# Optimization experiments

Measured on AMD Instinct MI355X. Metric: run time of the kernel, lower is better.

The kernel has to match this reference:

```python
import jax, jax.numpy as jnp
import numpy as np

EPS = 1e-6
NEG_SLOPE = 0.2


def knn_idx(xf, k):
    # xf: (B, C, N) flattened vector features; returns (B, N, k) neighbor indices
    xx = jnp.sum(xf * xf, axis=1)                       # (B, N)
    inner = jnp.einsum('bcn,bcm->bnm', xf, xf)          # (B, N, N)
    neg_dist = 2.0 * inner - xx[:, :, None] - xx[:, None, :]  # -||xi-xj||^2
    _, idx = jax.lax.top_k(neg_dist, k)                 # includes self (dist 0)
    return idx


def get_graph_feature(x, k):
    # x: (B, D, 3, N) -> edge features (B, 2D, 3, N, k)
    B, D, _, N = x.shape
    idx = knn_idx(x.reshape(B, D * 3, N), k)            # (B, N, k)
    pts = jnp.transpose(x, (0, 3, 1, 2))                # (B, N, D, 3)
    neigh = jax.vmap(lambda p, i: p[i])(pts, idx)       # (B, N, k, D, 3) gather
    center = jnp.broadcast_to(pts[:, :, None], neigh.shape)
    feat = jnp.concatenate([neigh - center, center], axis=3)  # (B, N, k, 2D, 3)
    return jnp.transpose(feat, (0, 3, 4, 1, 2))


def vn_linear_leakyrelu(x, Wf, Wd):
    # Vector-Neuron linear + leaky ReLU. x: (B, Cin, 3, ...),
    # Wf: (Cout, Cin), Wd: (Cout, Cin) or (1, Cin) when nonlinearity is shared.
    p = jnp.einsum('oi,bi...->bo...', Wf, x)
    d = jnp.einsum('oi,bi...->bo...', Wd, x)
    dot = jnp.sum(p * d, axis=2, keepdims=True)
    dsq = jnp.sum(d * d, axis=2, keepdims=True)
    proj = p - (dot / (dsq + EPS)) * d
    return NEG_SLOPE * p + (1.0 - NEG_SLOPE) * jnp.where(dot >= 0, p, proj)


def setup_inputs() -> dict:
    key = jax.random.key(0)
    ks = jax.random.split(key, 11)
    B, N = 8, 1024
    x = jax.random.normal(ks[0], (B, 3, N), dtype=jnp.float32)
    # dims = [1, 21, 21, 42, 85, 341]
    ins = [2, 42, 42, 84, 169]      # 2*dim_in for edge layers; sum(dims[1:-1]) for last
    outs = [21, 21, 42, 85, 341]
    dirs = [21, 21, 42, 85, 1]      # last layer has share_nonlinearity=True
    d = {"x": x}
    for i, (ci, co, cd) in enumerate(zip(ins, outs, dirs)):
        s = 1.0 / np.sqrt(ci)
        kf, kd = jax.random.split(ks[1 + i])
        d[f"Wf{i}"] = (jax.random.normal(kf, (co, ci), dtype=jnp.float32) * s)
        d[f"Wd{i}"] = (jax.random.normal(kd, (cd, ci), dtype=jnp.float32) * s)
    d["k"] = 20
    return d


def reference(x, Wf0, Wd0, Wf1, Wd1, Wf2, Wd2, Wf3, Wd3, Wf4, Wd4, k):
    cur = x[:, None]                 # (B, 1, 3, N)
    feats = []
    for Wf, Wd in ((Wf0, Wd0), (Wf1, Wd1), (Wf2, Wd2), (Wf3, Wd3)):
        g = get_graph_feature(cur, k)        # (B, 2D, 3, N, k)
        h = vn_linear_leakyrelu(g, Wf, Wd)   # (B, Dout, 3, N, k)
        cur = h.mean(axis=-1)                # mean over neighbors -> (B, Dout, 3, N)
        feats.append(cur)
    xcat = jnp.concatenate(feats, axis=1)    # (B, 169, 3, N)
    out = vn_linear_leakyrelu(xcat, Wf4, Wd4)
    return out.mean(axis=-1)                 # mean over points -> (B, 341, 3)
```

## Files before the change

kernel.cpp:

```cpp
#include <hip/hip_runtime.h>
#include <cstddef>

#define BB 8
#define NN 1024
#define KK 20
#define CCAT 169
#define NT 16
#define WTLD 384

template <int F>
__global__ __launch_bounds__(256) void dist_tile_kernel(
    const float* __restrict__ src, int bs, float* __restrict__ dist) {
  __shared__ float As[2][8][128];
  __shared__ float Bs[2][8][128];
  int b = blockIdx.z;
  int n0 = blockIdx.y * 128;
  int m0 = blockIdx.x * 128;
  int t = threadIdx.x;
  int tx = t & 15, ty = t >> 4;
  const float* p = src + (size_t)b * bs;

  float acc[8][8];
  float xn[8], xm[8];
#pragma unroll
  for (int i = 0; i < 8; ++i) {
    xn[i] = 0.f;
    xm[i] = 0.f;
#pragma unroll
    for (int j = 0; j < 8; ++j) acc[i][j] = 0.f;
  }

  int fr = t >> 5;
  int cc = (t & 31) << 2;
  constexpr int T = (F + 7) / 8;

  float4 av = {0.f, 0.f, 0.f, 0.f}, bv = {0.f, 0.f, 0.f, 0.f};
  if (fr < F) {
    av = *(const float4*)(p + (size_t)fr * NN + n0 + cc);
    bv = *(const float4*)(p + (size_t)fr * NN + m0 + cc);
  }
  *(float4*)&As[0][fr][cc] = av;
  *(float4*)&Bs[0][fr][cc] = bv;

#pragma unroll 1
  for (int k = 0; k < T; ++k) {
    __syncthreads();
    if (k + 1 < T) {
      int f = (k + 1) * 8 + fr;
      av = make_float4(0.f, 0.f, 0.f, 0.f);
      bv = make_float4(0.f, 0.f, 0.f, 0.f);
      if (f < F) {
        av = *(const float4*)(p + (size_t)f * NN + n0 + cc);
        bv = *(const float4*)(p + (size_t)f * NN + m0 + cc);
      }
    }
    const float(*A)[128] = As[k & 1];
    const float(*B)[128] = Bs[k & 1];
#pragma unroll
    for (int f2 = 0; f2 < 8; ++f2) {
      float4 al = *(const float4*)&A[f2][ty << 2];
      float4 ah = *(const float4*)&A[f2][64 + (ty << 2)];
      float4 bl = *(const float4*)&B[f2][tx << 2];
      float4 bh = *(const float4*)&B[f2][64 + (tx << 2)];
      float a[8] = {al.x, al.y, al.z, al.w, ah.x, ah.y, ah.z, ah.w};
      float bb[8] = {bl.x, bl.y, bl.z, bl.w, bh.x, bh.y, bh.z, bh.w};
#pragma unroll
      for (int i = 0; i < 8; ++i) xn[i] += a[i] * a[i];
#pragma unroll
      for (int j = 0; j < 8; ++j) xm[j] += bb[j] * bb[j];
#pragma unroll
      for (int i = 0; i < 8; ++i)
#pragma unroll
        for (int j = 0; j < 8; ++j) acc[i][j] += a[i] * bb[j];
    }
    if (k + 1 < T) {
      *(float4*)&As[(k + 1) & 1][fr][cc] = av;
      *(float4*)&Bs[(k + 1) & 1][fr][cc] = bv;
    }
  }

#pragma unroll
  for (int i = 0; i < 8; ++i)
#pragma unroll
    for (int j = 0; j < 8; ++j) acc[i][j] = 2.f * acc[i][j] - xn[i] - xm[j];

#pragma unroll
  for (int i = 0; i < 8; ++i) {
    int n = n0 + ((i < 4) ? ((ty << 2) + i) : (64 + (ty << 2) + i - 4));
    float* dr = dist + (((size_t)b * NN + n) << 10);
    *(float4*)(dr + m0 + (tx << 2)) =
        make_float4(acc[i][0], acc[i][1], acc[i][2], acc[i][3]);
    *(float4*)(dr + m0 + 64 + (tx << 2)) =
        make_float4(acc[i][4], acc[i][5], acc[i][6], acc[i][7]);
  }
}

__global__ __launch_bounds__(256) void topk_kernel(
    const float* __restrict__ dist, int* __restrict__ idx_out) {
  __shared__ unsigned long long q[4][16][64];
  int wave = threadIdx.x >> 6;
  int lane = threadIdx.x & 63;
  int row = blockIdx.x * 4 + wave;
  const float* d = dist + ((size_t)row << 10);

  unsigned long long key[16];
  {
    const float4* dp = (const float4*)(d + (lane << 4));
#pragma unroll
    for (int qd = 0; qd < 4; ++qd) {
      float4 v4 = dp[qd];
      float vv[4] = {v4.x, v4.y, v4.z, v4.w};
#pragma unroll
      for (int e = 0; e < 4; ++e) {
        int m = (lane << 4) + (qd << 2) + e;
        unsigned u = __float_as_uint(vv[e]);
        u = (u & 0x80000000u) ? ~u : (u | 0x80000000u);
        key[(qd << 2) + e] =
            ((unsigned long long)u << 32) | (unsigned)(NN - 1 - m);
      }
    }
  }

#pragma unroll
  for (int size = 2; size <= 16; size <<= 1) {
#pragma unroll
    for (int stride = size >> 1; stride > 0; stride >>= 1) {
#pragma unroll
      for (int i = 0; i < 16; ++i) {
        int j = i ^ stride;
        if (j > i) {
          unsigned long long a = key[i], c = key[j];
          bool desc = ((i & size) == 0);
          bool sw = desc ? (a < c) : (a > c);
          key[i] = sw ? c : a;
          key[j] = sw ? a : c;
        }
      }
    }
  }

#pragma unroll
  for (int s = 1; s < 16; ++s) q[wave][s - 1][lane] = key[s];
  q[wave][15][lane] = 0ull;

  int* out = idx_out + row * KK;
  unsigned long long head = key[0];
  int ptr = 0;
  for (int r = 0; r < KK; ++r) {
    unsigned hv = (unsigned)(head >> 32);
    unsigned v = hv;
#pragma unroll
    for (int off = 32; off > 0; off >>= 1) {
      unsigned o = __shfl_xor(v, off, 64);
      v = (o > v) ? o : v;
    }
    unsigned long long tie = __ballot(hv == v);
    unsigned il;
    if (tie & (tie - 1)) {
      unsigned c = (hv == v) ? (unsigned)head : 0u;
#pragma unroll
      for (int off = 32; off > 0; off >>= 1) {
        unsigned o = __shfl_xor(c, off, 64);
        c = (o > c) ? o : c;
      }
      il = c;
    } else {
      int wl = __builtin_ctzll(tie);
      il = __shfl((unsigned)head, wl, 64);
    }
    if (lane == 0) out[r] = (NN - 1) - (int)il;
    if (hv == v && (unsigned)head == il) {
      head = q[wave][ptr][lane];
      ++ptr;
    }
  }
}

template <int DD>
__global__ __launch_bounds__(256) void edge_fused_kernel(
    const float* __restrict__ src, int bs, int Co, int nsplit,
    const float* __restrict__ Wf, const float* __restrict__ Wd,
    const int* __restrict__ idx, int ooff, float* __restrict__ xcat) {
  __shared__ float2 Ulds[3 * NN];
  __shared__ float2 Vlds[3 * NN];
  __shared__ float4 Wlds[48];
  int bo = blockIdx.x;
  int b = bo / Co, o = bo % Co;
  int t = threadIdx.x;

  if (t < DD) {
    float wfa = Wf[o * 2 * DD + t];
    float wfb = Wf[o * 2 * DD + DD + t] - wfa;
    float wda = Wd[o * 2 * DD + t];
    float wdb = Wd[o * 2 * DD + DD + t] - wda;
    Wlds[t] = make_float4(wfa, wfb, wda, wdb);
  }
  __syncthreads();

  const float* sb = src + (size_t)b * bs;
  {
    int c0 = t << 2;
    float4 uf[3], vf[3], ud[3], vd[3];
#pragma unroll
    for (int r = 0; r < 3; ++r) {
      uf[r] = make_float4(0.f, 0.f, 0.f, 0.f);
      vf[r] = make_float4(0.f, 0.f, 0.f, 0.f);
      ud[r] = make_float4(0.f, 0.f, 0.f, 0.f);
      vd[r] = make_float4(0.f, 0.f, 0.f, 0.f);
    }
#pragma unroll 2
    for (int i = 0; i < DD; ++i) {
      const float* row = sb + (size_t)i * 3 * NN + c0;
      float4 s[3];
      s[0] = *(const float4*)(row);
      s[1] = *(const float4*)(row + 1024);
      s[2] = *(const float4*)(row + 2048);
      float4 w = Wlds[i];
#pragma unroll
      for (int r = 0; r < 3; ++r) {
        uf[r].x += w.x * s[r].x; uf[r].y += w.x * s[r].y;
        uf[r].z += w.x * s[r].z; uf[r].w += w.x * s[r].w;
        vf[r].x += w.y * s[r].x; vf[r].y += w.y * s[r].y;
        vf[r].z += w.y * s[r].z; vf[r].w += w.y * s[r].w;
        ud[r].x += w.z * s[r].x; ud[r].y += w.z * s[r].y;
        ud[r].z += w.z * s[r].z; ud[r].w += w.z * s[r].w;
        vd[r].x += w.w * s[r].x; vd[r].y += w.w * s[r].y;
        vd[r].z += w.w * s[r].z; vd[r].w += w.w * s[r].w;
      }
    }
#pragma unroll
    for (int r = 0; r < 3; ++r) {
      int g = t + 256 * r;
      *(float4*)&Ulds[(g << 2) + 0] =
          make_float4(uf[r].x, ud[r].x, uf[r].y, ud[r].y);
      *(float4*)&Ulds[(g << 2) + 2] =
          make_float4(uf[r].z, ud[r].z, uf[r].w, ud[r].w);
      *(float4*)&Vlds[(g << 2) + 0] =
          make_float4(vf[r].x, vd[r].x, vf[r].y, vd[r].y);
      *(float4*)&Vlds[(g << 2) + 2] =
          make_float4(vf[r].z, vd[r].z, vf[r].w, vd[r].w);
    }
  }
  __syncthreads();

  const float inv_k = 1.f / KK;
  int cnt = NN / nsplit;
  int nbase = blockIdx.y * cnt;
  for (int n = nbase + t; n < nbase + cnt; n += 256) {
    float2 v0 = Vlds[n];
    float2 v1 = Vlds[NN + n];
    float2 v2 = Vlds[2 * NN + n];
    const int4* ip = (const int4*)(idx + (b * NN + n) * KK);
    float a0 = 0.f, a1 = 0.f, a2 = 0.f;
#pragma unroll
    for (int qq = 0; qq < 5; ++qq) {
      int4 iv = ip[qq];
      int nbs[4] = {iv.x, iv.y, iv.z, iv.w};
#pragma unroll
      for (int jj = 0; jj < 4; ++jj) {
        int nb = nbs[jj];
        float2 u0 = Ulds[nb];
        float2 u1 = Ulds[NN + nb];
        float2 u2 = Ulds[2 * NN + nb];
        float pf0 = u0.x + v0.x, pd0 = u0.y + v0.y;
        float pf1 = u1.x + v1.x, pd1 = u1.y + v1.y;
        float pf2 = u2.x + v2.x, pd2 = u2.y + v2.y;
        float dot = pf0 * pd0 + pf1 * pd1 + pf2 * pd2;
        float dsq = pd0 * pd0 + pd1 * pd1 + pd2 * pd2;
        float g = (dot >= 0.f) ? 0.f : 0.8f * dot / (dsq + 1e-6f);
        a0 += pf0 - g * pd0;
        a1 += pf1 - g * pd1;
        a2 += pf2 - g * pd2;
      }
    }
    size_t ob = (size_t)b * CCAT * 3 * NN + (size_t)(ooff + o) * 3 * NN + n;
    xcat[ob] = a0 * inv_k;
    xcat[ob + NN] = a1 * inv_k;
    xcat[ob + 2 * NN] = a2 * inv_k;
  }
}

__global__ __launch_bounds__(256) void prep_kernel(
    const float* __restrict__ Wf4, float* __restrict__ Wt,
    float* __restrict__ zpad) {
  int o = blockIdx.x * 256 + threadIdx.x;
  int f = blockIdx.y;
  if (o < WTLD)
    Wt[(size_t)f * WTLD + o] = (f < CCAT && o < 341) ? Wf4[o * CCAT + f] : 0.f;
  if (blockIdx.x == 0 && blockIdx.y == 0) zpad[threadIdx.x] = 0.f;
}

__device__ __forceinline__ void gl2lds16(const float* g, float* l) {
  __builtin_amdgcn_global_load_lds(
      (const __attribute__((address_space(1))) unsigned int*)g,
      (__attribute__((address_space(3))) unsigned int*)l, 16, 0, 0);
}

__global__ __launch_bounds__(256) void final_fused_kernel(
    const float* __restrict__ xcat, const float* __restrict__ Wt,
    const float* __restrict__ Wd4, const float* __restrict__ zpad,
    float* __restrict__ part) {
  __shared__ float Ws[2][16][64];
  __shared__ float Xs[2][3][16][64];
  __shared__ float Wda[176];
  int b = blockIdx.z;
  int o0 = blockIdx.y * 64;
  int n0 = blockIdx.x * 64;
  int t = threadIdx.x;
  int tx = t & 15, ty = t >> 4;

  if (t < 176) Wda[t] = (t < CCAT) ? Wd4[t] : 0.f;

  float acc[3][4][4];
  float dv[3][4];
#pragma unroll
  for (int c = 0; c < 3; ++c) {
#pragma unroll
    for (int i = 0; i < 4; ++i)
#pragma unroll
      for (int j = 0; j < 4; ++j) acc[c][i][j] = 0.f;
#pragma unroll
    for (int j = 0; j < 4; ++j) dv[c][j] = 0.f;
  }

  const float* xb = xcat + (size_t)b * CCAT * 3 * NN;
  const int NTILE = 11;

  {
    const float* wsrc = Wt + (size_t)ty * WTLD + o0 + (tx << 2);
    gl2lds16(wsrc, &Ws[0][ty][tx << 2]);
#pragma unroll
    for (int c = 0; c < 3; ++c) {
      const float* xsrc = xb + ((size_t)ty * 3 + c) * NN + n0 + (tx << 2);
      gl2lds16(xsrc, &Xs[0][c][ty][tx << 2]);
    }
  }

#pragma unroll 1
  for (int tt = 0; tt < NTILE; ++tt) {
    int buf = tt & 1;
    __syncthreads();
    if (tt + 1 < NTILE) {
      int f = (tt + 1) * 16 + ty;
      const float* wsrc = Wt + (size_t)f * WTLD + o0 + (tx << 2);
      gl2lds16(wsrc, &Ws[buf ^ 1][ty][tx << 2]);
#pragma unroll
      for (int c = 0; c < 3; ++c) {
        const float* xsrc = (f < CCAT)
                                ? xb + ((size_t)f * 3 + c) * NN + n0 + (tx << 2)
                                : zpad + (tx << 2);
        gl2lds16(xsrc, &Xs[buf ^ 1][c][ty][tx << 2]);
      }
    }
#pragma unroll
    for (int f2 = 0; f2 < 16; ++f2) {
      float4 w = *(const float4*)&Ws[buf][f2][ty << 2];
      float wa[4] = {w.x, w.y, w.z, w.w};
      float wd = Wda[tt * 16 + f2];
#pragma unroll
      for (int c = 0; c < 3; ++c) {
        float4 x = *(const float4*)&Xs[buf][c][f2][tx << 2];
        float xa[4] = {x.x, x.y, x.z, x.w};
#pragma unroll
        for (int j = 0; j < 4; ++j) dv[c][j] += wd * xa[j];
#pragma unroll
        for (int i = 0; i < 4; ++i)
#pragma unroll
          for (int j = 0; j < 4; ++j) acc[c][i][j] += wa[i] * xa[j];
      }
    }
  }

  float s[3][4];
#pragma unroll
  for (int c = 0; c < 3; ++c)
#pragma unroll
    for (int i = 0; i < 4; ++i) s[c][i] = 0.f;
#pragma unroll
  for (int i = 0; i < 4; ++i) {
#pragma unroll
    for (int j = 0; j < 4; ++j) {
      float d0 = dv[0][j], d1 = dv[1][j], d2 = dv[2][j];
      float p0 = acc[0][i][j], p1 = acc[1][i][j], p2 = acc[2][i][j];
      float dot = p0 * d0 + p1 * d1 + p2 * d2;
      float dsq = d0 * d0 + d1 * d1 + d2 * d2;
      float g = (dot >= 0.f) ? 0.f : 0.8f * dot / (dsq + 1e-6f);
      s[0][i] += p0 - g * d0;
      s[1][i] += p1 - g * d1;
      s[2][i] += p2 - g * d2;
    }
  }

#pragma unroll
  for (int off = 1; off < 16; off <<= 1) {
#pragma unroll
    for (int c = 0; c < 3; ++c)
#pragma unroll
      for (int i = 0; i < 4; ++i) s[c][i] += __shfl_xor(s[c][i], off, 64);
  }
  if (tx == 0) {
#pragma unroll
    for (int i = 0; i < 4; ++i) {
      int o = o0 + (ty << 2) + i;
      if (o < 341) {
#pragma unroll
        for (int c = 0; c < 3; ++c)
          part[(((size_t)b * 341 + o) * 3 + c) * NT + blockIdx.x] = s[c][i];
      }
    }
  }
}

__global__ void final_reduce_kernel(const float* __restrict__ part,
                                    float* __restrict__ out) {
  int t = blockIdx.x * 256 + threadIdx.x;
  if (t >= BB * 341 * 3) return;
  const float* p = part + (size_t)t * NT;
  float s = 0.f;
#pragma unroll
  for (int nt = 0; nt < NT; ++nt) s += p[nt];
  out[t] = s * (1.f / 1024.f);
}

extern "C" void kernel_launch(void* const* d_in, const int* in_sizes, int n_in,
                              void* d_out, int out_size, void* d_ws,
                              size_t ws_size, hipStream_t stream) {
  (void)in_sizes; (void)n_in; (void)out_size; (void)ws_size;
  const float* x = (const float*)d_in[0];
  const float* Wf[5] = {(const float*)d_in[1], (const float*)d_in[3],
                        (const float*)d_in[5], (const float*)d_in[7],
                        (const float*)d_in[9]};
  const float* Wd[5] = {(const float*)d_in[2], (const float*)d_in[4],
                        (const float*)d_in[6], (const float*)d_in[8],
                        (const float*)d_in[10]};

  float* ws = (float*)d_ws;
  float* dist = ws;
  float* part = ws;
  float* Wt = ws + 262144;
  float* zpad = Wt + 176 * WTLD;
  size_t off = (size_t)BB * NN * NN;
  int* idx = (int*)(ws + off);
  off += (size_t)BB * NN * KK;
  float* xcat = ws + off;

  struct LayerCfg { int D, Co, inoff, ooff, nsplit; };
  const LayerCfg L[4] = {
      {1, 21, 0, 0, 4},
      {21, 21, 0, 21, 4},
      {21, 42, 21, 42, 2},
      {42, 85, 42, 84, 1},
  };

  for (int l = 0; l < 4; ++l) {
    const float* src = (l == 0) ? x : (xcat + (size_t)L[l].inoff * 3 * NN);
    int bs = (l == 0) ? 3 * NN : CCAT * 3 * NN;
    int D = L[l].D, Co = L[l].Co;

    dim3 dg(8, 8, BB);
    if (D == 1)
      dist_tile_kernel<3><<<dg, 256, 0, stream>>>(src, bs, dist);
    else if (D == 21)
      dist_tile_kernel<63><<<dg, 256, 0, stream>>>(src, bs, dist);
    else
      dist_tile_kernel<126><<<dg, 256, 0, stream>>>(src, bs, dist);

    topk_kernel<<<(BB * NN) / 4, 256, 0, stream>>>(dist, idx);

    dim3 eg(BB * Co, L[l].nsplit);
    if (D == 1)
      edge_fused_kernel<1><<<eg, 256, 0, stream>>>(
          src, bs, Co, L[l].nsplit, Wf[l], Wd[l], idx, L[l].ooff, xcat);
    else if (D == 21)
      edge_fused_kernel<21><<<eg, 256, 0, stream>>>(
          src, bs, Co, L[l].nsplit, Wf[l], Wd[l], idx, L[l].ooff, xcat);
    else
      edge_fused_kernel<42><<<eg, 256, 0, stream>>>(
          src, bs, Co, L[l].nsplit, Wf[l], Wd[l], idx, L[l].ooff, xcat);
  }

  prep_kernel<<<dim3(2, 176), 256, 0, stream>>>(Wf[4], Wt, zpad);
  final_fused_kernel<<<dim3(NT, 6, BB), 256, 0, stream>>>(xcat, Wt, Wd[4],
                                                          zpad, part);
  final_reduce_kernel<<<(BB * 341 * 3 + 255) / 256, 256, 0, stream>>>(
      part, (float*)d_out);
}
```

Before: 394.9 us.

## Fuse layer-0 distance and top-k into one kernel; repack edge LDS layout

For the first layer (3-dim input), a new knn3 kernel computes pairwise distances directly from LDS-resident points and runs the top-k selection in place. This removes the 32 MB distance-matrix write and re-read and one kernel launch for that layer. Separately, the edge kernel's LDS storage is repacked from three float2 arrays into a float4 plus a float2 per point, so each neighbor gather needs two LDS loads instead of three. Each block in the new kernel recomputes the distances for its four rows, which adds some redundant ALU work, and the float4 layout may change LDS bank-conflict behavior.

```diff
diff --git a/kernel.cpp b/kernel.cpp
--- a/kernel.cpp
+++ b/kernel.cpp
@@ -95,32 +95,9 @@
   }
 }
 
-__global__ __launch_bounds__(256) void topk_kernel(
-    const float* __restrict__ dist, int* __restrict__ idx_out) {
-  __shared__ unsigned long long q[4][16][64];
-  int wave = threadIdx.x >> 6;
-  int lane = threadIdx.x & 63;
-  int row = blockIdx.x * 4 + wave;
-  const float* d = dist + ((size_t)row << 10);
-
-  unsigned long long key[16];
-  {
-    const float4* dp = (const float4*)(d + (lane << 4));
-#pragma unroll
-    for (int qd = 0; qd < 4; ++qd) {
-      float4 v4 = dp[qd];
-      float vv[4] = {v4.x, v4.y, v4.z, v4.w};
-#pragma unroll
-      for (int e = 0; e < 4; ++e) {
-        int m = (lane << 4) + (qd << 2) + e;
-        unsigned u = __float_as_uint(vv[e]);
-        u = (u & 0x80000000u) ? ~u : (u | 0x80000000u);
-        key[(qd << 2) + e] =
-            ((unsigned long long)u << 32) | (unsigned)(NN - 1 - m);
-      }
-    }
-  }
-
+__device__ __forceinline__ void topk_core(
+    unsigned long long key[16], unsigned long long (*q)[64], int lane,
+    int* out) {
 #pragma unroll
   for (int size = 2; size <= 16; size <<= 1) {
 #pragma unroll
@@ -140,10 +117,9 @@
   }
 
 #pragma unroll
-  for (int s = 1; s < 16; ++s) q[wave][s - 1][lane] = key[s];
-  q[wave][15][lane] = 0ull;
-
-  int* out = idx_out + row * KK;
+  for (int s = 1; s < 16; ++s) q[s - 1][lane] = key[s];
+  q[15][lane] = 0ull;
+
   unsigned long long head = key[0];
   int ptr = 0;
   for (int r = 0; r < KK; ++r) {
@@ -170,10 +146,70 @@
     }
     if (lane == 0) out[r] = (NN - 1) - (int)il;
     if (hv == v && (unsigned)head == il) {
-      head = q[wave][ptr][lane];
+      head = q[ptr][lane];
       ++ptr;
     }
   }
+}
+
+__device__ __forceinline__ unsigned long long mk_key(float val, int m) {
+  unsigned u = __float_as_uint(val);
+  u = (u & 0x80000000u) ? ~u : (u | 0x80000000u);
+  return ((unsigned long long)u << 32) | (unsigned)(NN - 1 - m);
+}
+
+__global__ __launch_bounds__(256) void topk_kernel(
+    const float* __restrict__ dist, int* __restrict__ idx_out) {
+  __shared__ unsigned long long q[4][16][64];
+  int wave = threadIdx.x >> 6;
+  int lane = threadIdx.x & 63;
+  int row = blockIdx.x * 4 + wave;
+  const float* d = dist + ((size_t)row << 10);
+
+  unsigned long long key[16];
+  {
+    const float4* dp = (const float4*)(d + (lane << 4));
+#pragma unroll
+    for (int qd = 0; qd < 4; ++qd) {
+      float4 v4 = dp[qd];
+      float vv[4] = {v4.x, v4.y, v4.z, v4.w};
+#pragma unroll
+      for (int e = 0; e < 4; ++e)
+        key[(qd << 2) + e] = mk_key(vv[e], (lane << 4) + (qd << 2) + e);
+    }
+  }
+  topk_core(key, q[wave], lane, idx_out + row * KK);
+}
+
+__global__ __launch_bounds__(256) void knn3_kernel(
+    const float* __restrict__ src, int* __restrict__ idx_out) {
+  __shared__ float xl[3 * NN];
+  __shared__ unsigned long long q[4][16][64];
+  int b = blockIdx.y;
+  int t = threadIdx.x;
+  int wave = t >> 6;
+  int lane = t & 63;
+  int n = blockIdx.x * 4 + wave;
+  const float* sb = src + (size_t)b * 3 * NN;
+
+#pragma unroll
+  for (int r = 0; r < 3; ++r)
+    ((float4*)xl)[t + 256 * r] = ((const float4*)sb)[t + 256 * r];
+  __syncthreads();
+
+  float xn0 = xl[n], xn1 = xl[NN + n], xn2 = xl[2 * NN + n];
+  float xnn = xn0 * xn0 + xn1 * xn1 + xn2 * xn2;
+
+  unsigned long long key[16];
+#pragma unroll
+  for (int s = 0; s < 16; ++s) {
+    int m = lane + (s << 6);
+    float xm0 = xl[m], xm1 = xl[NN + m], xm2 = xl[2 * NN + m];
+    float dot = xn0 * xm0 + xn1 * xm1 + xn2 * xm2;
+    float xmn = xm0 * xm0 + xm1 * xm1 + xm2 * xm2;
+    key[s] = mk_key(2.f * dot - xnn - xmn, m);
+  }
+  topk_core(key, q[wave], lane, idx_out + ((size_t)b * NN + n) * KK);
 }
 
 template <int DD>
@@ -181,8 +217,10 @@
     const float* __restrict__ src, int bs, int Co, int nsplit,
     const float* __restrict__ Wf, const float* __restrict__ Wd,
     const int* __restrict__ idx, int ooff, float* __restrict__ xcat) {
-  __shared__ float2 Ulds[3 * NN];
-  __shared__ float2 Vlds[3 * NN];
+  __shared__ float4 UA[NN];
+  __shared__ float2 UB2[NN];
+  __shared__ float4 VA[NN];
+  __shared__ float2 VB2[NN];
   __shared__ float4 Wlds[48];
   int bo = blockIdx.x;
   int b = bo / Co, o = bo % Co;
@@ -200,45 +238,40 @@
   const float* sb = src + (size_t)b * bs;
   {
     int c0 = t << 2;
-    float4 uf[3], vf[3], ud[3], vd[3];
-#pragma unroll
-    for (int r = 0; r < 3; ++r) {
-      uf[r] = make_float4(0.f, 0.f, 0.f, 0.f);
-      vf[r] = make_float4(0.f, 0.f, 0.f, 0.f);
-      ud[r] = make_float4(0.f, 0.f, 0.f, 0.f);
-      vd[r] = make_float4(0.f, 0.f, 0.f, 0.f);
-    }
+    float uf[3][4], vf[3][4], ud[3][4], vd[3][4];
+#pragma unroll
+    for (int r = 0; r < 3; ++r)
+#pragma unroll
+      for (int e = 0; e < 4; ++e) {
+        uf[r][e] = 0.f; vf[r][e] = 0.f; ud[r][e] = 0.f; vd[r][e] = 0.f;
+      }
 #pragma unroll 2
     for (int i = 0; i < DD; ++i) {
       const float* row = sb + (size_t)i * 3 * NN + c0;
-      float4 s[3];
-      s[0] = *(const float4*)(row);
-      s[1] = *(const float4*)(row + 1024);
-      s[2] = *(const float4*)(row + 2048);
+      float4 s0 = *(const float4*)(row);
+      float4 s1 = *(const float4*)(row + 1024);
+      float4 s2 = *(const float4*)(row + 2048);
+      float se[3][4] = {{s0.x, s0.y, s0.z, s0.w},
+                        {s1.x, s1.y, s1.z, s1.w},
+                        {s2.x, s2.y, s2.z, s2.w}};
       float4 w = Wlds[i];
 #pragma unroll
-      for (int r = 0; r < 3; ++r) {
-        uf[r].x += w.x * s[r].x; uf[r].y += w.x * s[r].y;
-        uf[r].z += w.x * s[r].z; uf[r].w += w.x * s[r].w;
-        vf[r].x += w.y * s[r].x; vf[r].y += w.y * s[r].y;
-        vf[r].z += w.y * s[r].z; vf[r].w += w.y * s[r].w;
-        ud[r].x += w.z * s[r].x; ud[r].y += w.z * s[r].y;
-        ud[r].z += w.z * s[r].z; ud[r].w += w.z * s[r].w;
-        vd[r].x += w.w * s[r].x; vd[r].y += w.w * s[r].y;
-        vd[r].z += w.w * s[r].z; vd[r].w += w.w * s[r].w;
-      }
-    }
-#pragma unroll
-    for (int r = 0; r < 3; ++r) {
-      int g = t + 256 * r;
-      *(float4*)&Ulds[(g << 2) + 0] =
-          make_float4(uf[r].x, ud[r].x, uf[r].y, ud[r].y);
-      *(float4*)&Ulds[(g << 2) + 2] =
-          make_float4(uf[r].z, ud[r].z, uf[r].w, ud[r].w);
-      *(float4*)&Vlds[(g << 2) + 0] =
-          make_float4(vf[r].x, vd[r].x, vf[r].y, vd[r].y);
-      *(float4*)&Vlds[(g << 2) + 2] =
-          make_float4(vf[r].z, vd[r].z, vf[r].w, vd[r].w);
+      for (int r = 0; r < 3; ++r)
+#pragma unroll
+        for (int e = 0; e < 4; ++e) {
+          uf[r][e] += w.x * se[r][e];
+          vf[r][e] += w.y * se[r][e];
+          ud[r][e] += w.z * se[r][e];
+          vd[r][e] += w.w * se[r][e];
+        }
+    }
+#pragma unroll
+    for (int e = 0; e < 4; ++e) {
+      int n = (t << 2) + e;
+      UA[n] = make_float4(uf[0][e], ud[0][e], uf[1][e], ud[1][e]);
+      UB2[n] = make_float2(uf[2][e], ud[2][e]);
+      VA[n] = make_float4(vf[0][e], vd[0][e], vf[1][e], vd[1][e]);
+      VB2[n] = make_float2(vf[2][e], vd[2][e]);
     }
   }
   __syncthreads();
@@ -247,9 +280,8 @@
   int cnt = NN / nsplit;
   int nbase = blockIdx.y * cnt;
   for (int n = nbase + t; n < nbase + cnt; n += 256) {
-    float2 v0 = Vlds[n];
-    float2 v1 = Vlds[NN + n];
-    float2 v2 = Vlds[2 * NN + n];
+    float4 va = VA[n];
+    float2 vb = VB2[n];
     const int4* ip = (const int4*)(idx + (b * NN + n) * KK);
     float a0 = 0.f, a1 = 0.f, a2 = 0.f;
 #pragma unroll
@@ -259,12 +291,11 @@
 #pragma unroll
       for (int jj = 0; jj < 4; ++jj) {
         int nb = nbs[jj];
-        float2 u0 = Ulds[nb];
-        float2 u1 = Ulds[NN + nb];
-        float2 u2 = Ulds[2 * NN + nb];
-        float pf0 = u0.x + v0.x, pd0 = u0.y + v0.y;
-        float pf1 = u1.x + v1.x, pd1 = u1.y + v1.y;
-        float pf2 = u2.x + v2.x, pd2 = u2.y + v2.y;
+        float4 ua = UA[nb];
+        float2 ub = UB2[nb];
+        float pf0 = ua.x + va.x, pd0 = ua.y + va.y;
+        float pf1 = ua.z + va.z, pd1 = ua.w + va.w;
+        float pf2 = ub.x + vb.x, pd2 = ub.y + vb.y;
         float dot = pf0 * pd0 + pf1 * pd1 + pf2 * pd2;
         float dsq = pd0 * pd0 + pd1 * pd1 + pd2 * pd2;
         float g = (dot >= 0.f) ? 0.f : 0.8f * dot / (dsq + 1e-6f);
@@ -457,15 +488,16 @@
     int bs = (l == 0) ? 3 * NN : CCAT * 3 * NN;
     int D = L[l].D, Co = L[l].Co;
 
-    dim3 dg(8, 8, BB);
-    if (D == 1)
-      dist_tile_kernel<3><<<dg, 256, 0, stream>>>(src, bs, dist);
-    else if (D == 21)
-      dist_tile_kernel<63><<<dg, 256, 0, stream>>>(src, bs, dist);
-    else
-      dist_tile_kernel<126><<<dg, 256, 0, stream>>>(src, bs, dist);
-
-    topk_kernel<<<(BB * NN) / 4, 256, 0, stream>>>(dist, idx);
+    if (l == 0) {
+      knn3_kernel<<<dim3(NN / 4, BB), 256, 0, stream>>>(x, idx);
+    } else {
+      dim3 dg(8, 8, BB);
+      if (D == 21)
+        dist_tile_kernel<63><<<dg, 256, 0, stream>>>(src, bs, dist);
+      else
+        dist_tile_kernel<126><<<dg, 256, 0, stream>>>(src, bs, dist);
+      topk_kernel<<<(BB * NN) / 4, 256, 0, stream>>>(dist, idx);
+    }
 
     dim3 eg(BB * Co, L[l].nsplit);
     if (D == 1)
```

Result: no change. 390.7 us, median of 2 (-1.1%).
